# Kernel optimization log

Measured on AMD Instinct MI355X. Metric: run time of the kernel, lower is better.

The kernel has to match this reference:

```python
import jax, jax.numpy as jnp
import numpy as np

B, K, R = 16, 256, 256          # batch, text length, encoder dim (r_out_size)
CONV_OUT = 8                    # l_conv_out_size
SW_C = 16                       # l_swish_c_out_size
SW_W = 16                       # l_swish_w_out_size
KS = 3                          # l_conv_kernel_size
T_MAX = 1000                    # torch.clamp(pred_mel_len, max=1000) -> static frame dim
BN_EPS = 1e-5
LN_EPS = 1e-5


def _layer_norm(x, g, b):
    mu = jnp.mean(x, -1, keepdims=True)
    var = jnp.var(x, -1, keepdims=True)
    return (x - mu) * jax.lax.rsqrt(var + LN_EPS) * g + b


def _conv_block(V, w, b, bn_g, bn_b, ln_g, ln_b):
    # ConvBlock: Conv1d(SAME) -> eval BatchNorm (running mean 0 / var 1) -> SiLU -> LayerNorm
    x = jax.lax.conv_general_dilated(V, w, (1,), "SAME",
                                     dimension_numbers=("NWC", "WIO", "NWC")) + b
    x = x * (bn_g / jnp.sqrt(1.0 + BN_EPS)) + bn_b
    x = jax.nn.silu(x)
    return _layer_norm(x, ln_g, ln_b)


def _swish_block(S, E, V8, w1, b1, w2, b2):
    # SwishBlock: Linear(concat([S,E,V8], -1)) -> SiLU -> Linear -> SiLU,
    # without materializing the [B,T,K,CONV_OUT+2] concat (split the first matmul).
    base = V8 @ w1[2:] + b1                                           # [B,K,H]
    h = jax.nn.silu(S[..., None] * w1[0] + E[..., None] * w1[1] + base[:, None])  # [B,T,K,H]
    return jax.nn.silu(h @ w2 + b2)


def setup_inputs():
    key = jax.random.key(0)
    ks = jax.random.split(key, 20)
    f32 = jnp.float32

    inp = {}
    # durations ~ U[0,10): per-utterance sum ~1280 >> T_MAX, so every length clamps to T_MAX
    inp["dur"] = jax.random.uniform(ks[0], (B, K), dtype=f32) * 10.0
    inp["V"] = jax.random.normal(ks[1], (B, K, R), dtype=f32)
    inp["pos_text"] = jnp.tile(jnp.arange(K, dtype=jnp.int32)[None], (B, 1))
    inp["text_mask"] = jnp.zeros((B, K), dtype=bool)

    def n(k, shape, s):
        return jax.random.normal(k, shape, dtype=f32) * s

    for tag, i in (("c", 2), ("w", 6)):
        inp[f"conv_{tag}_w"] = n(ks[i], (KS, R, CONV_OUT), 0.05)
        inp[f"conv_{tag}_b"] = jnp.zeros((CONV_OUT,), f32)
        inp[f"bn_{tag}_g"] = jnp.ones((CONV_OUT,), f32)
        inp[f"bn_{tag}_b"] = jnp.zeros((CONV_OUT,), f32)
        inp[f"ln_{tag}_g"] = jnp.ones((CONV_OUT,), f32)
        inp[f"ln_{tag}_b"] = jnp.zeros((CONV_OUT,), f32)
    inp["swc_w1"] = n(ks[10], (CONV_OUT + 2, SW_C), 0.3)
    inp["swc_b1"] = jnp.zeros((SW_C,), f32)
    inp["swc_w2"] = n(ks[11], (SW_C, SW_C), 0.3)
    inp["swc_b2"] = jnp.zeros((SW_C,), f32)
    inp["sww_w1"] = n(ks[12], (CONV_OUT + 2, SW_W), 0.3)
    inp["sww_b1"] = jnp.zeros((SW_W,), f32)
    inp["sww_w2"] = n(ks[13], (SW_W, SW_W), 0.3)
    inp["sww_b2"] = jnp.zeros((SW_W,), f32)
    inp["proj_w_w"] = n(ks[14], (SW_W, 1), 0.3)
    inp["proj_w_b"] = jnp.zeros((1,), f32)
    inp["lin_e_w"] = n(ks[15], (SW_C, R), 0.1)
    inp["lin_e_b"] = jnp.zeros((R,), f32)
    inp["ln_o_g"] = jnp.ones((R,), f32)
    inp["ln_o_b"] = jnp.zeros((R,), f32)
    return inp


def reference(dur, V, pos_text, text_mask,
              conv_c_w, conv_c_b, bn_c_g, bn_c_b, ln_c_g, ln_c_b,
              conv_w_w, conv_w_b, bn_w_g, bn_w_b, ln_w_g, ln_w_b,
              swc_w1, swc_b1, swc_w2, swc_b2,
              sww_w1, sww_b1, sww_w2, sww_b2,
              proj_w_w, proj_w_b, lin_e_w, lin_e_b, ln_o_g, ln_o_b):
    pred_mel_len = jnp.minimum(jnp.round(dur.sum(-1)), T_MAX).astype(jnp.int32)  # [B]
    pred_mel_mask = jnp.arange(T_MAX, dtype=jnp.int32)[None, :] >= pred_mel_len[:, None]  # [B,T]
    tm = text_mask[:, None, :]       # [B,1,K]
    mm = pred_mel_mask[:, :, None]   # [B,T,1]
    attn_mask = tm | mm              # [B,T,K]

    e_k = jnp.cumsum(dur, axis=1)    # token end boundaries   [B,K]
    s_k = e_k - dur                  # token start boundaries [B,K]
    t = jnp.arange(1, T_MAX + 1, dtype=dur.dtype)[None, :, None]   # frame index [1,T,1]
    S = jnp.where(attn_mask, 0.0, t - s_k[:, None, :])             # [B,T,K]
    E = jnp.where(attn_mask, 0.0, e_k[:, None, :] - t)             # [B,T,K]

    Vw = _conv_block(V, conv_w_w, conv_w_b, bn_w_g, bn_w_b, ln_w_g, ln_w_b)
    Wh = _swish_block(S, E, Vw, sww_w1, sww_b1, sww_w2, sww_b2)    # [B,T,K,SW_W]
    logits = jnp.squeeze(Wh @ proj_w_w, -1) + proj_w_b[0]          # [B,T,K]
    logits = jnp.where(tm, -jnp.inf, logits)
    W = jax.nn.softmax(logits, axis=2)
    W = jnp.where(mm, 0.0, W)

    Vc = _conv_block(V, conv_c_w, conv_c_b, bn_c_g, bn_c_b, ln_c_g, ln_c_b)
    C = _swish_block(S, E, Vc, swc_w1, swc_b1, swc_w2, swc_b2)     # [B,T,K,SW_C]

    agg = jnp.einsum("btk,btkp->btp", W, C)                        # [B,T,SW_C]
    up = jnp.matmul(W, V) + (agg @ lin_e_w + lin_e_b)              # [B,T,R]
    up = _layer_norm(up, ln_o_g, ln_o_b)
    up = jnp.where(pred_mel_mask[..., None], 0.0, up)
    return up, pred_mel_mask, pred_mel_len, W
```

## Files before the change

kernel.cpp:

```cpp
#include <hip/hip_runtime.h>
#include <cstddef>

constexpr int Bn = 16, Kn = 256, Rn = 256, Tn = 1000, C8 = 8, SW = 16;
constexpr size_t UP_SZ    = (size_t)Bn * Tn * Rn;
constexpr size_t MASK_OFF = UP_SZ;
constexpr size_t LEN_OFF  = MASK_OFF + (size_t)Bn * Tn;
constexpr size_t W_OFF    = LEN_OFF + Bn;

using half4_t = __attribute__((ext_vector_type(4))) _Float16;
using f32x4_t = __attribute__((ext_vector_type(4))) float;
using uint2_t = __attribute__((ext_vector_type(2))) unsigned int;

__device__ __forceinline__ float fast_rcp(float x) { return __builtin_amdgcn_rcpf(x); }
__device__ __forceinline__ float fast_exp2(float x) { return __builtin_amdgcn_exp2f(x); }
constexpr float LOG2E = 1.44269504088896340736f;
__device__ __forceinline__ float silu_f(float x) {
    return x * fast_rcp(1.f + fast_exp2(-LOG2E * x));
}

__global__ __launch_bounds__(256) void conv_partial_kernel(
    const float* __restrict__ V,
    const float* __restrict__ wW, const float* __restrict__ wC,
    float* __restrict__ part)
{
    const int rc = blockIdx.x, b = blockIdx.y, k = threadIdx.x;
    constexpr int RPAD = 33;
    __shared__ float vt[258 * RPAD];
    if (k < 16) {
        const int row = (k < 8) ? 0 : 257;
        const int j = (k & 7) * 4;
        vt[row * RPAD + j] = 0.f; vt[row * RPAD + j + 1] = 0.f;
        vt[row * RPAD + j + 2] = 0.f; vt[row * RPAD + j + 3] = 0.f;
    }
    const float* vsrc = V + ((size_t)(b * Kn + k)) * Rn + rc * 32;
#pragma unroll
    for (int j = 0; j < 8; j++) {
        const float4 qv = *(const float4*)(vsrc + j * 4);
        float* dst = &vt[(k + 1) * RPAD + j * 4];
        dst[0] = qv.x; dst[1] = qv.y; dst[2] = qv.z; dst[3] = qv.w;
    }
    __syncthreads();

    float aw[C8], ac[C8];
#pragma unroll
    for (int c = 0; c < C8; c++) { aw[c] = 0.f; ac[c] = 0.f; }
    for (int dk = 0; dk < 3; dk++) {
        const float* wp = wW + (size_t)(dk * Rn + rc * 32) * C8;
        const float* cp = wC + (size_t)(dk * Rn + rc * 32) * C8;
        const float* vrow = &vt[(k + dk) * RPAD];
#pragma unroll 4
        for (int r = 0; r < 32; r++) {
            const float v = vrow[r];
#pragma unroll
            for (int c = 0; c < C8; c++) {
                aw[c] = fmaf(v, wp[r * C8 + c], aw[c]);
                ac[c] = fmaf(v, cp[r * C8 + c], ac[c]);
            }
        }
    }
    float* dst = part + ((size_t)(b * 8 + rc) * Kn + k) * 16;
    *(float4*)(dst + 0)  = make_float4(aw[0], aw[1], aw[2], aw[3]);
    *(float4*)(dst + 4)  = make_float4(aw[4], aw[5], aw[6], aw[7]);
    *(float4*)(dst + 8)  = make_float4(ac[0], ac[1], ac[2], ac[3]);
    *(float4*)(dst + 12) = make_float4(ac[4], ac[5], ac[6], ac[7]);
}

__device__ __forceinline__ void conv_post(
    const float* acc, const float* cb, const float* bng, const float* bnb,
    const float* lng, const float* lnb, const float* w1, const float* b1,
    float* __restrict__ dst)
{
    const float bnscale = rsqrtf(1.f + 1e-5f);
    float x[C8];
    float mu = 0.f;
#pragma unroll
    for (int c = 0; c < C8; c++) {
        float v = (acc[c] + cb[c]) * (bng[c] * bnscale) + bnb[c];
        v = silu_f(v);
        x[c] = v; mu += v;
    }
    mu *= (1.f / C8);
    float var = 0.f;
#pragma unroll
    for (int c = 0; c < C8; c++) { float dd = x[c] - mu; var += dd * dd; }
    var *= (1.f / C8);
    const float rs = rsqrtf(var + 1e-5f);
    float y[C8];
#pragma unroll
    for (int c = 0; c < C8; c++) y[c] = (x[c] - mu) * rs * lng[c] + lnb[c];
#pragma unroll
    for (int c2 = 0; c2 < SW; c2++) {
        float a = b1[c2];
#pragma unroll
        for (int p = 0; p < C8; p++) a = fmaf(y[p], w1[(2 + p) * SW + c2], a);
        dst[c2] = a;
    }
}

__global__ __launch_bounds__(256) void conv_scan_finish_kernel(
    const float* __restrict__ dur,
    const float* __restrict__ part,
    const unsigned char* __restrict__ tmask_g,
    const float* __restrict__ bW, const float* __restrict__ bngW, const float* __restrict__ bnbW,
    const float* __restrict__ lngW, const float* __restrict__ lnbW,
    const float* __restrict__ bC, const float* __restrict__ bngC, const float* __restrict__ bnbC,
    const float* __restrict__ lngC, const float* __restrict__ lnbC,
    const float* __restrict__ sww_w1, const float* __restrict__ sww_b1,
    const float* __restrict__ swc_w1, const float* __restrict__ swc_b1,
    float* __restrict__ alpha_ws, float* __restrict__ ab_ws,
    int* __restrict__ len_ws, float* __restrict__ out)
{
    const int b = blockIdx.x, k = threadIdx.x;
    __shared__ float sc[Kn];
    const float d = dur[b * Kn + k];
    sc[k] = d;
    __syncthreads();
    for (int off = 1; off < Kn; off <<= 1) {
        float v = (k >= off) ? sc[k - off] : 0.f;
        __syncthreads();
        sc[k] += v;
        __syncthreads();
    }
    const float ek = sc[k];
    const float sk = ek - d;
    const float total = sc[Kn - 1];
    int len = (int)rintf(total);
    if (len > Tn) len = Tn;
    if (k == 0) { len_ws[b] = len; out[LEN_OFF + b] = (float)len; }
    for (int t = k; t < Tn; t += 256)
        out[MASK_OFF + (size_t)b * Tn + t] = (t >= len) ? 1.f : 0.f;
    if (b == 0 && k < 16) {
        alpha_ws[k]      = sww_w1[k] - sww_w1[SW + k];
        alpha_ws[16 + k] = swc_w1[k] - swc_w1[SW + k];
    }

    float aw[C8], ac[C8];
#pragma unroll
    for (int c = 0; c < C8; c++) { aw[c] = 0.f; ac[c] = 0.f; }
#pragma unroll 2
    for (int rc = 0; rc < 8; rc++) {
        const float4* p = (const float4*)(part + ((size_t)(b * 8 + rc) * Kn + k) * 16);
        const float4 q0 = p[0], q1 = p[1], q2 = p[2], q3 = p[3];
        aw[0] += q0.x; aw[1] += q0.y; aw[2] += q0.z; aw[3] += q0.w;
        aw[4] += q1.x; aw[5] += q1.y; aw[6] += q1.z; aw[7] += q1.w;
        ac[0] += q2.x; ac[1] += q2.y; ac[2] += q2.z; ac[3] += q2.w;
        ac[4] += q3.x; ac[5] += q3.y; ac[6] += q3.z; ac[7] += q3.w;
    }
    float basew[SW], basec[SW];
    conv_post(aw, bW, bngW, bnbW, lngW, lnbW, sww_w1, sww_b1, basew);
    conv_post(ac, bC, bngC, bnbC, lngC, lnbC, swc_w1, swc_b1, basec);

    const bool msk = tmask_g[b * Kn + k] != 0;
    float* dst = ab_ws + ((size_t)(b * Kn) + k) * 32;
#pragma unroll
    for (int c = 0; c < SW; c++) {
        const float w0w = sww_w1[c], w1w_ = sww_w1[SW + c];
        const float w0c = swc_w1[c], w1c_ = swc_w1[SW + c];
        dst[c]      = msk ? basew[c] : fmaf(ek, w1w_, fmaf(-sk, w0w, basew[c]));
        dst[16 + c] = msk ? basec[c] : fmaf(ek, w1c_, fmaf(-sk, w0c, basec[c]));
    }
}

__global__ __launch_bounds__(256) void logits_kernel(
    const unsigned char* __restrict__ tm, const int* __restrict__ len_ws,
    const float* __restrict__ alpha_ws, const float* __restrict__ ab_ws,
    const float* __restrict__ sww_w2, const float* __restrict__ sww_b2,
    const float* __restrict__ proj_w, const float* __restrict__ proj_b,
    const float* __restrict__ swc_w2, const float* __restrict__ swc_b2,
    float* __restrict__ agg_ws, float* __restrict__ out)
{
    const int t0 = blockIdx.x * 4, b = blockIdx.y, tid = threadIdx.x;
    const int lane = tid & 63, w = tid >> 6, q = lane >> 4, m = lane & 15;
    const int len = len_ws[b];

    __shared__ __align__(16) unsigned int hA[256 * 10];
    __shared__ __align__(16) unsigned int hB[256 * 10];
    __shared__ __align__(16) unsigned int hC[256 * 10];
    __shared__ float red[8];
    __shared__ __align__(16) float aggw[2][4][16];

    float bw[16], bc[16];
    {
        const float4* bp = (const float4*)(ab_ws + (((size_t)b * Kn) + tid) * 32);
#pragma unroll
        for (int i = 0; i < 4; i++) {
            const float4 v = bp[i];
            bw[4*i] = v.x; bw[4*i+1] = v.y; bw[4*i+2] = v.z; bw[4*i+3] = v.w;
        }
#pragma unroll
        for (int i = 0; i < 4; i++) {
            const float4 v = bp[4 + i];
            bc[4*i] = v.x; bc[4*i+1] = v.y; bc[4*i+2] = v.z; bc[4*i+3] = v.w;
        }
    }
    const float mk = (tm[b * Kn + tid] != 0) ? 0.f : 1.f;

    half4_t AWhi, AWlo, ACf;
    float pj[4], b2wv[4], b2cv[4], mb[4];
#pragma unroll
    for (int i = 0; i < 4; i++) {
        const int c = 4 * q + i;
        const float vw = sww_w2[c * SW + m];
        const _Float16 hi = (_Float16)vw;
        AWhi[i] = hi;
        AWlo[i] = (_Float16)(vw - (float)hi);
        ACf[i]  = (_Float16)(swc_w2[c * SW + m]);
        pj[i]   = proj_w[c];
        b2wv[i] = sww_b2[c];
        b2cv[i] = swc_b2[c];
        mb[i]   = (tm[b * Kn + 64 * w + 16 * i + m] != 0) ? -INFINITY : 0.f;
    }
    const float pb = proj_b[0];

    int pend = -1, pendpar = 0;

    for (int ti = 0; ti < 4; ti++) {
        const int t = t0 + ti;
        float* __restrict__ W_out = out + W_OFF + ((size_t)b * Tn + t) * Kn;
        if (t >= len) { W_out[tid] = 0.f; continue; }
        const float u = (float)(t + 1);
        const float umk = u * mk;

#pragma unroll
        for (int p = 0; p < 8; p++) {
            const float x0 = fmaf(umk, alpha_ws[2*p],   bw[2*p]);
            const float x1 = fmaf(umk, alpha_ws[2*p+1], bw[2*p+1]);
            const float h0 = silu_f(x0), h1 = silu_f(x1);
            const auto hp = __builtin_amdgcn_cvt_pkrtz(h0, h1);
            hA[tid * 10 + p] = __builtin_bit_cast(unsigned int, hp);
            const float l0 = h0 - (float)hp.x, l1 = h1 - (float)hp.y;
            hB[tid * 10 + p] = __builtin_bit_cast(unsigned int,
                                __builtin_amdgcn_cvt_pkrtz(l0, l1));
            const float y0 = fmaf(umk, alpha_ws[16 + 2*p],   bc[2*p]);
            const float y1 = fmaf(umk, alpha_ws[16 + 2*p+1], bc[2*p+1]);
            hC[tid * 10 + p] = __builtin_bit_cast(unsigned int,
                                __builtin_amdgcn_cvt_pkrtz(silu_f(y0), silu_f(y1)));
        }

        f32x4_t o[4];
#pragma unroll
        for (int j = 0; j < 4; j++) {
            const int row = 64 * w + 16 * j + m;
            const uint2_t rh = *(const uint2_t*)&hA[row * 10 + 2 * q];
            const uint2_t rl = *(const uint2_t*)&hB[row * 10 + 2 * q];
            const half4_t bh = __builtin_bit_cast(half4_t, rh);
            const half4_t bl = __builtin_bit_cast(half4_t, rl);
            f32x4_t acc = {0.f, 0.f, 0.f, 0.f};
            acc = __builtin_amdgcn_mfma_f32_16x16x16f16(AWlo, bh, acc, 0, 0, 0);
            acc = __builtin_amdgcn_mfma_f32_16x16x16f16(AWhi, bl, acc, 0, 0, 0);
            acc = __builtin_amdgcn_mfma_f32_16x16x16f16(AWhi, bh, acc, 0, 0, 0);
            o[j] = acc;
        }

        float lg[4];
#pragma unroll
        for (int j = 0; j < 4; j++) {
            float s = silu_f(o[j][0] + b2wv[0]) * pj[0];
            s = fmaf(silu_f(o[j][1] + b2wv[1]), pj[1], s);
            s = fmaf(silu_f(o[j][2] + b2wv[2]), pj[2], s);
            s = fmaf(silu_f(o[j][3] + b2wv[3]), pj[3], s);
            s += __shfl_xor(s, 16, 64);
            s += __shfl_xor(s, 32, 64);
            lg[j] = s + pb + mb[j];
        }

        float mx = fmaxf(fmaxf(lg[0], lg[1]), fmaxf(lg[2], lg[3]));
#pragma unroll
        for (int off = 1; off <= 8; off <<= 1) mx = fmaxf(mx, __shfl_xor(mx, off, 64));
        if (lane == 0) red[w] = mx;
        __syncthreads();
        if (pend >= 0) {
            if (tid < 16)
                agg_ws[((size_t)b * Tn + pend) * 16 + tid] =
                    aggw[pendpar][0][tid] + aggw[pendpar][1][tid] +
                    aggw[pendpar][2][tid] + aggw[pendpar][3][tid];
            pend = -1;
        }
        const float M = fmaxf(fmaxf(red[0], red[1]), fmaxf(red[2], red[3]));
        float pex[4];
#pragma unroll
        for (int j = 0; j < 4; j++) pex[j] = fast_exp2(LOG2E * (lg[j] - M));
        float ssum = (pex[0] + pex[1]) + (pex[2] + pex[3]);
#pragma unroll
        for (int off = 1; off <= 8; off <<= 1) ssum += __shfl_xor(ssum, off, 64);
        if (lane == 0) red[4 + w] = ssum;
        __syncthreads();
        const float inv = fast_rcp(red[4] + red[5] + red[6] + red[7]);
        float wgt[4];
#pragma unroll
        for (int j = 0; j < 4; j++) wgt[j] = pex[j] * inv;
        if (q == 0) {
#pragma unroll
            for (int j = 0; j < 4; j++) W_out[64 * w + 16 * j + m] = wgt[j];
        }

        f32x4_t ap = {0.f, 0.f, 0.f, 0.f};
#pragma unroll
        for (int j = 0; j < 4; j++) {
            const int row = 64 * w + 16 * j + m;
            const uint2_t rc2 = *(const uint2_t*)&hC[row * 10 + 2 * q];
            f32x4_t zz = {0.f, 0.f, 0.f, 0.f};
            const f32x4_t oc = __builtin_amdgcn_mfma_f32_16x16x16f16(
                ACf, __builtin_bit_cast(half4_t, rc2), zz, 0, 0, 0);
#pragma unroll
            for (int i = 0; i < 4; i++)
                ap[i] = fmaf(silu_f(oc[i] + b2cv[i]), wgt[j], ap[i]);
        }
#pragma unroll
        for (int off = 1; off <= 8; off <<= 1) {
            ap[0] += __shfl_xor(ap[0], off, 64);
            ap[1] += __shfl_xor(ap[1], off, 64);
            ap[2] += __shfl_xor(ap[2], off, 64);
            ap[3] += __shfl_xor(ap[3], off, 64);
        }
        if (m == 0)
            *(float4*)&aggw[ti & 1][w][4 * q] = make_float4(ap[0], ap[1], ap[2], ap[3]);
        pend = t; pendpar = ti & 1;
    }
    if (pend >= 0) {
        __syncthreads();
        if (tid < 16)
            agg_ws[((size_t)b * Tn + pend) * 16 + tid] =
                aggw[pendpar][0][tid] + aggw[pendpar][1][tid] +
                aggw[pendpar][2][tid] + aggw[pendpar][3][tid];
    }
}

__global__ __launch_bounds__(256) void matvec_kernel(
    const float* __restrict__ V, const float* __restrict__ Wg,
    float* __restrict__ out)
{
    const int tb = blockIdx.x, rq = blockIdx.y, b = blockIdx.z;
    const int t0 = tb * 64, r0 = rq * 64;
    const int tid = threadIdx.x;
    __shared__ float4 Wl[64 * 32];
    __shared__ float4 Vl[128 * 16];

    const int tg = tid >> 4, rg = tid & 15;
    float4 acc[4];
#pragma unroll
    for (int i = 0; i < 4; i++) acc[i] = make_float4(0.f, 0.f, 0.f, 0.f);

    const float4* Wg4 = (const float4*)Wg;
    const float4* V4 = (const float4*)V;

    for (int kh = 0; kh < 2; kh++) {
        __syncthreads();
#pragma unroll
        for (int ch = 0; ch < 8; ch++) {
            const int idx = ch * 256 + tid;
            const int tt = idx >> 5, c4 = idx & 31;
            const int t = t0 + tt;
            Wl[idx] = (t < Tn) ? Wg4[(((size_t)b * Tn + t) * Kn >> 2) + kh * 32 + c4]
                               : make_float4(0.f, 0.f, 0.f, 0.f);
        }
#pragma unroll
        for (int ch = 0; ch < 8; ch++) {
            const int idx = ch * 256 + tid;
            const int k = idx >> 4, qq = idx & 15;
            Vl[idx] = V4[(((size_t)b * Kn + kh * 128 + k) * Rn >> 2) + (r0 >> 2) + qq];
        }
        __syncthreads();

        for (int k4 = 0; k4 < 32; k4++) {
            const float4 v0 = Vl[(k4 * 4 + 0) * 16 + rg];
            const float4 v1 = Vl[(k4 * 4 + 1) * 16 + rg];
            const float4 v2 = Vl[(k4 * 4 + 2) * 16 + rg];
            const float4 v3 = Vl[(k4 * 4 + 3) * 16 + rg];
#pragma unroll
            for (int i = 0; i < 4; i++) {
                const float4 wv = Wl[(tg * 4 + i) * 32 + k4];
                acc[i].x = fmaf(wv.x, v0.x, acc[i].x);
                acc[i].y = fmaf(wv.x, v0.y, acc[i].y);
                acc[i].z = fmaf(wv.x, v0.z, acc[i].z);
                acc[i].w = fmaf(wv.x, v0.w, acc[i].w);
                acc[i].x = fmaf(wv.y, v1.x, acc[i].x);
                acc[i].y = fmaf(wv.y, v1.y, acc[i].y);
                acc[i].z = fmaf(wv.y, v1.z, acc[i].z);
                acc[i].w = fmaf(wv.y, v1.w, acc[i].w);
                acc[i].x = fmaf(wv.z, v2.x, acc[i].x);
                acc[i].y = fmaf(wv.z, v2.y, acc[i].y);
                acc[i].z = fmaf(wv.z, v2.z, acc[i].z);
                acc[i].w = fmaf(wv.z, v2.w, acc[i].w);
                acc[i].x = fmaf(wv.w, v3.x, acc[i].x);
                acc[i].y = fmaf(wv.w, v3.y, acc[i].y);
                acc[i].z = fmaf(wv.w, v3.z, acc[i].z);
                acc[i].w = fmaf(wv.w, v3.w, acc[i].w);
            }
        }
    }

#pragma unroll
    for (int i = 0; i < 4; i++) {
        const int t = t0 + tg * 4 + i;
        if (t < Tn)
            *(float4*)(out + ((size_t)b * Tn + t) * Rn + r0 + rg * 4) = acc[i];
    }
}

__global__ __launch_bounds__(256) void ln_kernel(
    const float* __restrict__ agg_ws, const int* __restrict__ len_ws,
    const float* __restrict__ lin_e_w, const float* __restrict__ lin_e_b,
    const float* __restrict__ ln_o_g, const float* __restrict__ ln_o_b,
    float* __restrict__ out)
{
    const int b = blockIdx.y, tid = threadIdx.x;
    const int sub = tid >> 6, lane = tid & 63;
    const int t = blockIdx.x * 4 + sub;
    const int r0 = lane * 4;
    float* __restrict__ row = out + ((size_t)b * Tn + t) * Rn;
    const int len = len_ws[b];
    if (t >= len) {
        *(float4*)(row + r0) = make_float4(0.f, 0.f, 0.f, 0.f);
        return;
    }

    float4 acc = *(const float4*)(row + r0);
    {
        const float4 be = *(const float4*)(lin_e_b + r0);
        acc.x += be.x; acc.y += be.y; acc.z += be.z; acc.w += be.w;
    }
    const float* aggp = agg_ws + ((size_t)b * Tn + t) * 16;
#pragma unroll
    for (int p = 0; p < 16; p++) {
        const float a = aggp[p];
        const float4 l = *(const float4*)(lin_e_w + p * Rn + r0);
        acc.x = fmaf(a, l.x, acc.x); acc.y = fmaf(a, l.y, acc.y);
        acc.z = fmaf(a, l.z, acc.z); acc.w = fmaf(a, l.w, acc.w);
    }

    float s = (acc.x + acc.y) + (acc.z + acc.w);
#pragma unroll
    for (int off = 1; off <= 32; off <<= 1) s += __shfl_xor(s, off, 64);
    const float mu = s * (1.f / Rn);
    const float d0 = acc.x - mu, d1 = acc.y - mu, d2 = acc.z - mu, d3 = acc.w - mu;
    float vr = d0 * d0 + d1 * d1 + d2 * d2 + d3 * d3;
#pragma unroll
    for (int off = 1; off <= 32; off <<= 1) vr += __shfl_xor(vr, off, 64);
    const float rs = rsqrtf(vr * (1.f / Rn) + 1e-5f);

    const float4 g = *(const float4*)(ln_o_g + r0);
    const float4 bb = *(const float4*)(ln_o_b + r0);
    float4 res;
    res.x = d0 * rs * g.x + bb.x;
    res.y = d1 * rs * g.y + bb.y;
    res.z = d2 * rs * g.z + bb.z;
    res.w = d3 * rs * g.w + bb.w;
    *(float4*)(row + r0) = res;
}

extern "C" void kernel_launch(void* const* d_in, const int* in_sizes, int n_in,
                              void* d_out, int out_size, void* d_ws, size_t ws_size,
                              hipStream_t stream)
{
    const float* dur       = (const float*)d_in[0];
    const float* V         = (const float*)d_in[1];
    const unsigned char* text_mask = (const unsigned char*)d_in[3];
    const float* conv_c_w  = (const float*)d_in[4];
    const float* conv_c_b  = (const float*)d_in[5];
    const float* bn_c_g    = (const float*)d_in[6];
    const float* bn_c_b    = (const float*)d_in[7];
    const float* ln_c_g    = (const float*)d_in[8];
    const float* ln_c_b    = (const float*)d_in[9];
    const float* conv_w_w  = (const float*)d_in[10];
    const float* conv_w_b  = (const float*)d_in[11];
    const float* bn_w_g    = (const float*)d_in[12];
    const float* bn_w_b    = (const float*)d_in[13];
    const float* ln_w_g    = (const float*)d_in[14];
    const float* ln_w_b    = (const float*)d_in[15];
    const float* swc_w1    = (const float*)d_in[16];
    const float* swc_b1    = (const float*)d_in[17];
    const float* swc_w2    = (const float*)d_in[18];
    const float* swc_b2    = (const float*)d_in[19];
    const float* sww_w1    = (const float*)d_in[20];
    const float* sww_b1    = (const float*)d_in[21];
    const float* sww_w2    = (const float*)d_in[22];
    const float* sww_b2    = (const float*)d_in[23];
    const float* proj_w_w  = (const float*)d_in[24];
    const float* proj_w_b  = (const float*)d_in[25];
    const float* lin_e_w   = (const float*)d_in[26];
    const float* lin_e_b   = (const float*)d_in[27];
    const float* ln_o_g    = (const float*)d_in[28];
    const float* ln_o_b    = (const float*)d_in[29];

    float* out = (float*)d_out;
    float* wsf = (float*)d_ws;
    int*   len_ws   = (int*)wsf;
    float* alpha_ws = wsf + 64;
    float* ab_ws    = wsf + 128;
    float* scratch  = ab_ws + 131072;
    float* part     = scratch;
    float* agg_ws   = scratch;

    conv_partial_kernel<<<dim3(8, Bn), dim3(256), 0, stream>>>(V, conv_w_w, conv_c_w, part);
    conv_scan_finish_kernel<<<dim3(Bn), dim3(256), 0, stream>>>(
        dur, part, text_mask,
        conv_w_b, bn_w_g, bn_w_b, ln_w_g, ln_w_b,
        conv_c_b, bn_c_g, bn_c_b, ln_c_g, ln_c_b,
        sww_w1, sww_b1, swc_w1, swc_b1,
        alpha_ws, ab_ws, len_ws, out);
    logits_kernel<<<dim3(Tn / 4, Bn), dim3(256), 0, stream>>>(
        text_mask, len_ws, alpha_ws, ab_ws,
        sww_w2, sww_b2, proj_w_w, proj_w_b,
        swc_w2, swc_b2,
        agg_ws, out);
    matvec_kernel<<<dim3(16, 4, Bn), dim3(256), 0, stream>>>(
        V, out + W_OFF, out);
    ln_kernel<<<dim3(Tn / 4, Bn), dim3(256), 0, stream>>>(
        agg_ws, len_ws, lin_e_w, lin_e_b, ln_o_g, ln_o_b, out);
}
```

Before: 178.1 us.

## Compute W@V matmul with split-fp16 MFMA using pre-transposed V halves

Replaces the FP32 scalar-FMA W@V matmul with a 16x16x16 fp16 MFMA kernel. Precision is kept close to fp32 by splitting both operands into hi and lo fp16 parts and issuing three MFMAs per step. A new pre-pass transposes V and converts it to hi/lo fp16 arrays in workspace, and the W tile in LDS uses an XOR swizzle. This adds an extra kernel launch and a workspace write, and accuracy depends on the fp16 split, since small values in the lo part can underflow.

Measured after the change: 212.2 us. 19.1% more time.

```diff
diff --git a/kernel.cpp b/kernel.cpp
--- a/kernel.cpp
+++ b/kernel.cpp
@@ -63,6 +63,43 @@
     *(float4*)(dst + 4)  = make_float4(aw[4], aw[5], aw[6], aw[7]);
     *(float4*)(dst + 8)  = make_float4(ac[0], ac[1], ac[2], ac[3]);
     *(float4*)(dst + 12) = make_float4(ac[4], ac[5], ac[6], ac[7]);
+}
+
+__global__ __launch_bounds__(256) void vt_transpose_kernel(
+    const float* __restrict__ V,
+    unsigned short* __restrict__ vt_hi, unsigned short* __restrict__ vt_lo)
+{
+    const int kq = blockIdx.x, rq = blockIdx.y, b = blockIdx.z;
+    const int tid = threadIdx.x;
+    __shared__ float tile[64][65];
+    const int k0 = kq * 64, r0 = rq * 64;
+#pragma unroll
+    for (int ch = 0; ch < 4; ch++) {
+        const int idx = ch * 256 + tid;
+        const int kk = idx >> 4, c4 = (idx & 15) * 4;
+        const float4 v = *(const float4*)(V + ((size_t)(b * Kn) + k0 + kk) * Rn + r0 + c4);
+        tile[kk][c4] = v.x; tile[kk][c4 + 1] = v.y;
+        tile[kk][c4 + 2] = v.z; tile[kk][c4 + 3] = v.w;
+    }
+    __syncthreads();
+#pragma unroll
+    for (int ch = 0; ch < 4; ch++) {
+        const int idx = ch * 256 + tid;
+        const int rr = idx >> 4, k4 = (idx & 15) * 4;
+        const float v0 = tile[k4][rr], v1 = tile[k4 + 1][rr];
+        const float v2 = tile[k4 + 2][rr], v3 = tile[k4 + 3][rr];
+        const auto h01 = __builtin_amdgcn_cvt_pkrtz(v0, v1);
+        const auto h23 = __builtin_amdgcn_cvt_pkrtz(v2, v3);
+        uint2_t hi; hi.x = __builtin_bit_cast(unsigned int, h01);
+        hi.y = __builtin_bit_cast(unsigned int, h23);
+        const auto l01 = __builtin_amdgcn_cvt_pkrtz(v0 - (float)h01.x, v1 - (float)h01.y);
+        const auto l23 = __builtin_amdgcn_cvt_pkrtz(v2 - (float)h23.x, v3 - (float)h23.y);
+        uint2_t lo; lo.x = __builtin_bit_cast(unsigned int, l01);
+        lo.y = __builtin_bit_cast(unsigned int, l23);
+        const size_t off = (((size_t)b * Rn) + r0 + rr) * Kn + k0 + k4;
+        *(uint2_t*)&vt_hi[off] = hi;
+        *(uint2_t*)&vt_lo[off] = lo;
+    }
 }
 
 __device__ __forceinline__ void conv_post(
@@ -326,75 +363,74 @@
     }
 }
 
-__global__ __launch_bounds__(256) void matvec_kernel(
-    const float* __restrict__ V, const float* __restrict__ Wg,
+__global__ __launch_bounds__(256) void matvec_mfma_kernel(
+    const float* __restrict__ Wg,
+    const unsigned short* __restrict__ vt_hi, const unsigned short* __restrict__ vt_lo,
     float* __restrict__ out)
 {
     const int tb = blockIdx.x, rq = blockIdx.y, b = blockIdx.z;
-    const int t0 = tb * 64, r0 = rq * 64;
+    const int t0 = tb * 32, r0 = rq * 64;
     const int tid = threadIdx.x;
-    __shared__ float4 Wl[64 * 32];
-    __shared__ float4 Vl[128 * 16];
-
-    const int tg = tid >> 4, rg = tid & 15;
-    float4 acc[4];
-#pragma unroll
-    for (int i = 0; i < 4; i++) acc[i] = make_float4(0.f, 0.f, 0.f, 0.f);
+    const int lane = tid & 63, w = tid >> 6, q = lane >> 4, m = lane & 15;
+    __shared__ float4 Wl[32 * 64];
 
     const float4* Wg4 = (const float4*)Wg;
-    const float4* V4 = (const float4*)V;
-
-    for (int kh = 0; kh < 2; kh++) {
-        __syncthreads();
-#pragma unroll
-        for (int ch = 0; ch < 8; ch++) {
-            const int idx = ch * 256 + tid;
-            const int tt = idx >> 5, c4 = idx & 31;
-            const int t = t0 + tt;
-            Wl[idx] = (t < Tn) ? Wg4[(((size_t)b * Tn + t) * Kn >> 2) + kh * 32 + c4]
-                               : make_float4(0.f, 0.f, 0.f, 0.f);
-        }
-#pragma unroll
-        for (int ch = 0; ch < 8; ch++) {
-            const int idx = ch * 256 + tid;
-            const int k = idx >> 4, qq = idx & 15;
-            Vl[idx] = V4[(((size_t)b * Kn + kh * 128 + k) * Rn >> 2) + (r0 >> 2) + qq];
-        }
-        __syncthreads();
-
-        for (int k4 = 0; k4 < 32; k4++) {
-            const float4 v0 = Vl[(k4 * 4 + 0) * 16 + rg];
-            const float4 v1 = Vl[(k4 * 4 + 1) * 16 + rg];
-            const float4 v2 = Vl[(k4 * 4 + 2) * 16 + rg];
-            const float4 v3 = Vl[(k4 * 4 + 3) * 16 + rg];
-#pragma unroll
-            for (int i = 0; i < 4; i++) {
-                const float4 wv = Wl[(tg * 4 + i) * 32 + k4];
-                acc[i].x = fmaf(wv.x, v0.x, acc[i].x);
-                acc[i].y = fmaf(wv.x, v0.y, acc[i].y);
-                acc[i].z = fmaf(wv.x, v0.z, acc[i].z);
-                acc[i].w = fmaf(wv.x, v0.w, acc[i].w);
-                acc[i].x = fmaf(wv.y, v1.x, acc[i].x);
-                acc[i].y = fmaf(wv.y, v1.y, acc[i].y);
-                acc[i].z = fmaf(wv.y, v1.z, acc[i].z);
-                acc[i].w = fmaf(wv.y, v1.w, acc[i].w);
-                acc[i].x = fmaf(wv.z, v2.x, acc[i].x);
-                acc[i].y = fmaf(wv.z, v2.y, acc[i].y);
-                acc[i].z = fmaf(wv.z, v2.z, acc[i].z);
-                acc[i].w = fmaf(wv.z, v2.w, acc[i].w);
-                acc[i].x = fmaf(wv.w, v3.x, acc[i].x);
-                acc[i].y = fmaf(wv.w, v3.y, acc[i].y);
-                acc[i].z = fmaf(wv.w, v3.z, acc[i].z);
-                acc[i].w = fmaf(wv.w, v3.w, acc[i].w);
-            }
-        }
+#pragma unroll
+    for (int ch = 0; ch < 8; ch++) {
+        const int idx = ch * 256 + tid;
+        const int row = idx >> 6, sl = idx & 63;
+        const int t = t0 + row;
+        const float4 v = (t < Tn) ? Wg4[((size_t)b * Tn + t) * 64 + sl]
+                                  : make_float4(0.f, 0.f, 0.f, 0.f);
+        Wl[row * 64 + (sl ^ (row & 7))] = v;
+    }
+    __syncthreads();
+
+    const int tt = w & 1;
+    const int rp = w >> 1;
+    const int wrow = tt * 16 + m;
+    const size_t rbase0 = (((size_t)b * Rn) + r0 + rp * 32 + m) * Kn;
+    const size_t rbase1 = rbase0 + (size_t)16 * Kn;
+
+    f32x4_t acc0 = {0.f, 0.f, 0.f, 0.f};
+    f32x4_t acc1 = {0.f, 0.f, 0.f, 0.f};
+
+#pragma unroll
+    for (int ks = 0; ks < 16; ks++) {
+        const float4 wv = Wl[wrow * 64 + ((ks * 4 + q) ^ (wrow & 7))];
+        const auto h01 = __builtin_amdgcn_cvt_pkrtz(wv.x, wv.y);
+        const auto h23 = __builtin_amdgcn_cvt_pkrtz(wv.z, wv.w);
+        uint2_t uhi; uhi.x = __builtin_bit_cast(unsigned int, h01);
+        uhi.y = __builtin_bit_cast(unsigned int, h23);
+        const half4_t Ahi = __builtin_bit_cast(half4_t, uhi);
+        const auto l01 = __builtin_amdgcn_cvt_pkrtz(wv.x - (float)h01.x, wv.y - (float)h01.y);
+        const auto l23 = __builtin_amdgcn_cvt_pkrtz(wv.z - (float)h23.x, wv.w - (float)h23.y);
+        uint2_t ulo; ulo.x = __builtin_bit_cast(unsigned int, l01);
+        ulo.y = __builtin_bit_cast(unsigned int, l23);
+        const half4_t Alo = __builtin_bit_cast(half4_t, ulo);
+
+        const int koff = ks * 16 + 4 * q;
+        const half4_t Bh0 = __builtin_bit_cast(half4_t, *(const uint2_t*)&vt_hi[rbase0 + koff]);
+        const half4_t Bl0 = __builtin_bit_cast(half4_t, *(const uint2_t*)&vt_lo[rbase0 + koff]);
+        const half4_t Bh1 = __builtin_bit_cast(half4_t, *(const uint2_t*)&vt_hi[rbase1 + koff]);
+        const half4_t Bl1 = __builtin_bit_cast(half4_t, *(const uint2_t*)&vt_lo[rbase1 + koff]);
+
+        acc0 = __builtin_amdgcn_mfma_f32_16x16x16f16(Alo, Bh0, acc0, 0, 0, 0);
+        acc0 = __builtin_amdgcn_mfma_f32_16x16x16f16(Ahi, Bl0, acc0, 0, 0, 0);
+        acc0 = __builtin_amdgcn_mfma_f32_16x16x16f16(Ahi, Bh0, acc0, 0, 0, 0);
+        acc1 = __builtin_amdgcn_mfma_f32_16x16x16f16(Alo, Bh1, acc1, 0, 0, 0);
+        acc1 = __builtin_amdgcn_mfma_f32_16x16x16f16(Ahi, Bl1, acc1, 0, 0, 0);
+        acc1 = __builtin_amdgcn_mfma_f32_16x16x16f16(Ahi, Bh1, acc1, 0, 0, 0);
     }
 
 #pragma unroll
     for (int i = 0; i < 4; i++) {
-        const int t = t0 + tg * 4 + i;
-        if (t < Tn)
-            *(float4*)(out + ((size_t)b * Tn + t) * Rn + r0 + rg * 4) = acc[i];
+        const int t = t0 + tt * 16 + 4 * q + i;
+        if (t < Tn) {
+            float* rowp = out + ((size_t)b * Tn + t) * Rn + r0 + rp * 32 + m;
+            rowp[0]  = acc0[i];
+            rowp[16] = acc1[i];
+        }
     }
 }
 
@@ -491,7 +527,10 @@
     float* scratch  = ab_ws + 131072;
     float* part     = scratch;
     float* agg_ws   = scratch;
-
+    unsigned short* vt_hi = (unsigned short*)(scratch + 524288);
+    unsigned short* vt_lo = vt_hi + (size_t)Bn * Kn * Rn;
+
+    vt_transpose_kernel<<<dim3(4, 4, Bn), dim3(256), 0, stream>>>(V, vt_hi, vt_lo);
     conv_partial_kernel<<<dim3(8, Bn), dim3(256), 0, stream>>>(V, conv_w_w, conv_c_w, part);
     conv_scan_finish_kernel<<<dim3(Bn), dim3(256), 0, stream>>>(
         dur, part, text_mask,
@@ -504,8 +543,8 @@
         sww_w2, sww_b2, proj_w_w, proj_w_b,
         swc_w2, swc_b2,
         agg_ws, out);
-    matvec_kernel<<<dim3(16, 4, Bn), dim3(256), 0, stream>>>(
-        V, out + W_OFF, out);
+    matvec_mfma_kernel<<<dim3((Tn + 31) / 32, 4, Bn), dim3(256), 0, stream>>>(
+        out + W_OFF, vt_hi, vt_lo, out);
     ln_kernel<<<dim3(Tn / 4, Bn), dim3(256), 0, stream>>>(
         agg_ws, len_ws, lin_e_w, lin_e_b, ln_o_g, ln_o_b, out);
 }
```
